# Optimization experiments

Hardware: AMD Instinct MI355X
Metric: run time of the kernel (lower is better)

Reference implementation:

```python
import jax, jax.numpy as jnp
import numpy as np

N_NODES = 100000
IN_DIM = 128
HID_DIM = 128
N_EDGES = 1600000
BN_EPS = 1e-5


def setup_inputs() -> dict:
    key = jax.random.key(0)
    k1, k2, k3, k4 = jax.random.split(key, 4)
    x = jax.random.normal(k1, (N_NODES, IN_DIM), dtype=jnp.float32)
    edge_index = jax.random.randint(k2, (2, N_EDGES), 0, N_NODES, dtype=jnp.int64)
    # GCNConv linear weight (glorot) and bias
    W = jax.random.normal(k3, (HID_DIM, IN_DIM), dtype=jnp.float32) * (1.0 / np.sqrt(IN_DIM))
    b = jnp.zeros((HID_DIM,), dtype=jnp.float32)
    # BatchNorm affine params
    gamma = jnp.ones((HID_DIM,), dtype=jnp.float32)
    beta = jnp.zeros((HID_DIM,), dtype=jnp.float32)
    return {"x": x, "edge_index": edge_index, "W": W, "b": b, "gamma": gamma, "beta": beta}


def reference(x, edge_index, W, b, gamma, beta):
    n = x.shape[0]
    # --- GCNConv: add self loops, symmetric normalization ---
    loops = jnp.arange(n, dtype=edge_index.dtype)
    row = jnp.concatenate([edge_index[0], loops])  # source j
    col = jnp.concatenate([edge_index[1], loops])  # target i
    deg = jax.ops.segment_sum(jnp.ones_like(col, dtype=x.dtype), col, num_segments=n)
    deg_inv_sqrt = jnp.where(deg > 0, jax.lax.rsqrt(jnp.maximum(deg, 1e-12)), 0.0)
    norm = deg_inv_sqrt[row] * deg_inv_sqrt[col]  # [E+N]
    # linear transform then normalized gather-scatter aggregation
    h = x @ W.T  # [N, H]
    msgs = h[row] * norm[:, None]  # [E+N, H]
    out = jax.ops.segment_sum(msgs, col, num_segments=n) + b  # [N, H]
    # --- BatchNorm1d (training-mode batch stats, biased var) + ReLU ---
    mean = jnp.mean(out, axis=0)
    var = jnp.mean(jnp.square(out - mean), axis=0)
    out = (out - mean) * jax.lax.rsqrt(var + BN_EPS) * gamma + beta
    return jax.nn.relu(out)
```

## Files before the change

### kernel.cpp

```cpp
#include <hip/hip_runtime.h>

#define N_NODES 100000
#define N_EDGES 1600000
#define BN_EPS 1e-5f
#define NB 782
#define CAP 2688
#define CH 2048

typedef short short8 __attribute__((ext_vector_type(8)));
typedef float floatx4 __attribute__((ext_vector_type(4)));

__device__ __forceinline__ unsigned short f2bf(float f) {
    unsigned int u = __float_as_uint(f);
    unsigned int r = (u + 0x7fffu + ((u >> 16) & 1u)) >> 16;
    return (unsigned short)r;
}
__device__ __forceinline__ float bflo(unsigned int v) { return __uint_as_float(v << 16); }
__device__ __forceinline__ float bfhi(unsigned int v) { return __uint_as_float(v & 0xffff0000u); }

__global__ __launch_bounds__(256) void k_bin(const int* __restrict__ ei,
                                             int* __restrict__ bcnt,
                                             unsigned int* __restrict__ binned, int E) {
    __shared__ int hist[1024];
    __shared__ int base[1024];
    __shared__ int gbase[1024];
    __shared__ int warr[256];
    __shared__ unsigned int stage[CH];
    __shared__ unsigned short stb[CH];
    int tid = threadIdx.x;
    int e0 = blockIdx.x * CH;
    int cn = min(CH, E - e0);

    for (int i = tid; i < 1024; i += 256) hist[i] = 0;
    __syncthreads();

    unsigned int mycode[8];
    short myb[8], myslot[8];
    #pragma unroll
    for (int j = 0; j < 8; j++) {
        int idx = j * 256 + tid;
        if (idx < cn) {
            int e = e0 + idx;
            int src = ei[e];
            int dst = ei[E + e];
            int b = dst >> 7;
            mycode[j] = (unsigned int)src | ((unsigned int)(dst & 127) << 17);
            myb[j] = (short)b;
            myslot[j] = (short)atomicAdd(&hist[b], 1);
        } else myb[j] = -1;
    }
    __syncthreads();

    int h0 = hist[tid * 4], h1 = hist[tid * 4 + 1], h2 = hist[tid * 4 + 2], h3 = hist[tid * 4 + 3];
    int t4 = h0 + h1 + h2 + h3;
    warr[tid] = t4;
    __syncthreads();
    for (int o = 1; o < 256; o <<= 1) {
        int x = (tid >= o) ? warr[tid - o] : 0;
        __syncthreads();
        warr[tid] += x;
        __syncthreads();
    }
    int ex = warr[tid] - t4;
    base[tid * 4] = ex;
    base[tid * 4 + 1] = ex + h0;
    base[tid * 4 + 2] = ex + h0 + h1;
    base[tid * 4 + 3] = ex + h0 + h1 + h2;
    __syncthreads();

    #pragma unroll
    for (int j = 0; j < 8; j++) {
        if (myb[j] >= 0) {
            int p = base[myb[j]] + myslot[j];
            stage[p] = mycode[j];
            stb[p] = (unsigned short)myb[j];
        }
    }
    for (int b = tid; b < NB; b += 256) {
        int c = hist[b];
        if (c) gbase[b] = b * CAP + atomicAdd(&bcnt[b], c);
    }
    __syncthreads();
    for (int i = tid; i < cn; i += 256) {
        int b = stb[i];
        binned[gbase[b] + (i - base[b])] = stage[i];
    }
}

__global__ __launch_bounds__(256) void k_dd(const unsigned int* __restrict__ binned,
                                            const int* __restrict__ bcnt,
                                            float* __restrict__ dinv, int n) {
    __shared__ int hist[128];
    int b = blockIdx.x, t = threadIdx.x;
    int nb0 = b * 128;
    int e0 = b * CAP;
    int cnt = bcnt[b];
    if (t < 128) hist[t] = 0;
    __syncthreads();
    for (int i = t; i < cnt; i += 256)
        atomicAdd(&hist[binned[e0 + i] >> 17], 1);
    __syncthreads();
    int nr = min(128, n - nb0);
    if (t < nr) dinv[nb0 + t] = rsqrtf((float)(hist[t] + 1));
}

__global__ void k_wcvt(const float* __restrict__ Wf, unsigned short* __restrict__ Wb) {
    int i = blockIdx.x * 256 + threadIdx.x;
    if (i < 128 * 128) Wb[i] = f2bf(Wf[i]);
}

__global__ __launch_bounds__(256) void k_gemm(const float* __restrict__ x,
                                              const unsigned short* __restrict__ Wb,
                                              unsigned short* __restrict__ hb, int n) {
    int w = threadIdx.x >> 6;
    int l = threadIdx.x & 63;
    int rowbase = blockIdx.x * 256 + w * 64;
    int r16 = l & 15;
    int kg = l >> 4;

    short8 a[4][4];
    #pragma unroll
    for (int m = 0; m < 4; m++) {
        int row = rowbase + m * 16 + r16;
        int rca = min(row, n - 1);
        const float* base = x + rca * 128;
        #pragma unroll
        for (int q = 0; q < 4; q++) {
            const float4* xp = (const float4*)(base + q * 32 + kg * 8);
            float4 lo = xp[0], hi = xp[1];
            short8 af;
            af[0] = (short)f2bf(lo.x); af[1] = (short)f2bf(lo.y);
            af[2] = (short)f2bf(lo.z); af[3] = (short)f2bf(lo.w);
            af[4] = (short)f2bf(hi.x); af[5] = (short)f2bf(hi.y);
            af[6] = (short)f2bf(hi.z); af[7] = (short)f2bf(hi.w);
            a[m][q] = af;
        }
    }
    for (int t = 0; t < 8; t++) {
        int col = t * 16 + r16;
        short8 b[4];
        #pragma unroll
        for (int q = 0; q < 4; q++)
            b[q] = *(const short8*)(Wb + col * 128 + q * 32 + kg * 8);

        floatx4 acc[4] = {};
        #pragma unroll
        for (int m = 0; m < 4; m++)
            #pragma unroll
            for (int q = 0; q < 4; q++)
                acc[m] = __builtin_amdgcn_mfma_f32_16x16x32_bf16(a[m][q], b[q], acc[m], 0, 0, 0);

        #pragma unroll
        for (int m = 0; m < 4; m++) {
            #pragma unroll
            for (int r = 0; r < 4; r++) {
                int row = rowbase + m * 16 + kg * 4 + r;
                if (row < n) hb[row * 128 + col] = f2bf(acc[m][r]);
            }
        }
    }
}

__global__ __launch_bounds__(512) void k_fused(const unsigned int* __restrict__ hp,
        const float* __restrict__ dinv, const int* __restrict__ bcnt,
        const unsigned int* __restrict__ binned, float* __restrict__ out,
        float* __restrict__ sums, float* __restrict__ sumsq, int n) {
    __shared__ int hist[128], hsc[128];
    __shared__ float dl[128];
    __shared__ int sh_src[CAP];
    __shared__ float sh_nrm[CAP];
    __shared__ float ps[8][128], pq[8][128];
    int t = threadIdx.x;
    int w = t >> 6, l = t & 63;
    int b = blockIdx.x;
    int nb0 = b * 128;
    int e0 = b * CAP;
    int cnt = bcnt[b];
    int nr = min(128, n - nb0);

    if (t < 128) {
        hist[t] = 0;
        if (t < nr) dl[t] = dinv[nb0 + t];
    }
    __syncthreads();

    unsigned int mycode[6];
    short myslot[6];
    #pragma unroll
    for (int j = 0; j < 6; j++) {
        int i = j * 512 + t;
        if (i < cnt) {
            unsigned int code = binned[e0 + i];
            mycode[j] = code;
            myslot[j] = (short)atomicAdd(&hist[code >> 17], 1);
        } else myslot[j] = -1;
    }
    __syncthreads();

    int v = (t < 128) ? hist[t] : 0;
    if (t < 128) hsc[t] = v;
    __syncthreads();
    for (int o = 1; o < 128; o <<= 1) {
        int x = (t < 128 && t >= o) ? hsc[t - o] : 0;
        __syncthreads();
        if (t < 128) hsc[t] += x;
        __syncthreads();
    }

    #pragma unroll
    for (int j = 0; j < 6; j++) {
        if (myslot[j] >= 0) {
            unsigned int code = mycode[j];
            int ld = code >> 17;
            int src = code & 0x1FFFF;
            int pos = hsc[ld] - hist[ld] + myslot[j];
            sh_src[pos] = src;
            sh_nrm[pos] = dinv[src] * dl[ld];
        }
    }
    __syncthreads();

    float s0 = 0, s1 = 0, q0 = 0, q1 = 0;
    for (int r = w; r < nr; r += 8) {
        int i = nb0 + r;
        float di = dl[r];
        unsigned int sv = hp[i * 64 + l];
        float sn = di * di;
        float ax = bflo(sv) * sn;
        float ay = bfhi(sv) * sn;
        int off = hsc[r] - hist[r];
        int dg = hist[r];
        int e = 0;
        for (; e + 7 < dg; e += 8) {
            unsigned int hv[8]; float nn[8];
            #pragma unroll
            for (int j = 0; j < 8; j++) {
                int s = sh_src[off + e + j];
                nn[j] = sh_nrm[off + e + j];
                hv[j] = hp[s * 64 + l];
            }
            #pragma unroll
            for (int j = 0; j < 8; j++) {
                ax += nn[j] * bflo(hv[j]);
                ay += nn[j] * bfhi(hv[j]);
            }
        }
        for (; e < dg; e++) {
            int s = sh_src[off + e];
            float nnm = sh_nrm[off + e];
            unsigned int hv = hp[s * 64 + l];
            ax += nnm * bflo(hv);
            ay += nnm * bfhi(hv);
        }
        ((float2*)out)[i * 64 + l] = make_float2(ax, ay);
        s0 += ax; q0 += ax * ax;
        s1 += ay; q1 += ay * ay;
    }

    ps[w][2 * l] = s0; ps[w][2 * l + 1] = s1;
    pq[w][2 * l] = q0; pq[w][2 * l + 1] = q1;
    __syncthreads();
    if (t < 128) {
        float s = 0, q = 0;
        #pragma unroll
        for (int j = 0; j < 8; j++) { s += ps[j][t]; q += pq[j][t]; }
        atomicAdd(&sums[t], s);
        atomicAdd(&sumsq[t], q);
    }
}

__global__ void k_bn(float* __restrict__ out, const float* __restrict__ sums,
                     const float* __restrict__ sumsq, const float* __restrict__ gamma,
                     const float* __restrict__ beta, int n) {
    int idx = blockIdx.x * 256 + threadIdx.x;
    int total = n * 32;
    if (idx >= total) return;
    int c0 = (idx & 31) * 4;
    float invN = 1.0f / (float)n;
    float4 v = ((const float4*)out)[idx];
    float r[4] = {v.x, v.y, v.z, v.w};
    #pragma unroll
    for (int j = 0; j < 4; j++) {
        int c = c0 + j;
        float mean = sums[c] * invN;
        float var = sumsq[c] * invN - mean * mean;
        float scale = rsqrtf(var + BN_EPS) * gamma[c];
        float o = (r[j] - mean) * scale + beta[c];
        r[j] = fmaxf(o, 0.0f);
    }
    ((float4*)out)[idx] = make_float4(r[0], r[1], r[2], r[3]);
}

extern "C" void kernel_launch(void* const* d_in, const int* in_sizes, int n_in,
                              void* d_out, int out_size, void* d_ws, size_t ws_size,
                              hipStream_t stream) {
    const float* x     = (const float*)d_in[0];
    const int*   ei    = (const int*)d_in[1];
    const float* W     = (const float*)d_in[2];
    const float* gamma = (const float*)d_in[4];
    const float* beta  = (const float*)d_in[5];
    float* out = (float*)d_out;

    const int n = N_NODES, E = N_EDGES;

    unsigned short* hb   = (unsigned short*)d_ws;
    float* dinv   = (float*)(hb + 12800000);
    float* sums   = dinv + 100000;
    float* sumsq  = sums + 128;
    int*   bcnt   = (int*)(sumsq + 128);
    unsigned short* Wb = (unsigned short*)(bcnt + NB);
    unsigned int* binned = (unsigned int*)(Wb + 16384);

    hipMemsetAsync(sums, 0, (256 + NB) * sizeof(int), stream);

    k_bin<<<(E + CH - 1) / CH, 256, 0, stream>>>(ei, bcnt, binned, E);
    k_dd<<<NB, 256, 0, stream>>>(binned, bcnt, dinv, n);

    k_wcvt<<<64, 256, 0, stream>>>(W, Wb);
    k_gemm<<<(n + 255) / 256, 256, 0, stream>>>(x, Wb, hb, n);

    k_fused<<<NB, 512, 0, stream>>>((const unsigned int*)hb, dinv, bcnt, binned,
                                    out, sums, sumsq, n);

    k_bn<<<(n * 32 + 255) / 256, 256, 0, stream>>>(out, sums, sumsq, gamma, beta, n);
}
```

Measured before the change: 177.3 us.

## Halve destination bin size to 64 nodes and pack edge src/norm in LDS

Destination bins shrink from 128 to 64 nodes, doubling the block count for binning, degree and fused aggregation, and the fused kernel drops to 256 threads. The GEMM processes 128 rows per block instead of 256 to launch more blocks. Source index and norm are stored together as a uint2 in shared memory so each edge takes a single LDS load. The aim is more parallelism and lower LDS use per block for better occupancy, at the cost of a larger k_bin histogram/scan and a tighter per-bin capacity that could overflow.

Result: slower. 205.6 us (+16.0%).

```diff
diff --git a/kernel.cpp b/kernel.cpp
--- a/kernel.cpp
+++ b/kernel.cpp
@@ -3,8 +3,8 @@
 #define N_NODES 100000
 #define N_EDGES 1600000
 #define BN_EPS 1e-5f
-#define NB 782
-#define CAP 2688
+#define NB 1563
+#define CAP 1472
 #define CH 2048
 
 typedef short short8 __attribute__((ext_vector_type(8)));
@@ -21,9 +21,9 @@
 __global__ __launch_bounds__(256) void k_bin(const int* __restrict__ ei,
                                              int* __restrict__ bcnt,
                                              unsigned int* __restrict__ binned, int E) {
-    __shared__ int hist[1024];
-    __shared__ int base[1024];
-    __shared__ int gbase[1024];
+    __shared__ int hist[2048];
+    __shared__ int base[2048];
+    __shared__ int gbase[2048];
     __shared__ int warr[256];
     __shared__ unsigned int stage[CH];
     __shared__ unsigned short stb[CH];
@@ -31,7 +31,7 @@
     int e0 = blockIdx.x * CH;
     int cn = min(CH, E - e0);
 
-    for (int i = tid; i < 1024; i += 256) hist[i] = 0;
+    for (int i = tid; i < 2048; i += 256) hist[i] = 0;
     __syncthreads();
 
     unsigned int mycode[8];
@@ -43,17 +43,18 @@
             int e = e0 + idx;
             int src = ei[e];
             int dst = ei[E + e];
-            int b = dst >> 7;
-            mycode[j] = (unsigned int)src | ((unsigned int)(dst & 127) << 17);
+            int b = dst >> 6;
+            mycode[j] = (unsigned int)src | ((unsigned int)(dst & 63) << 17);
             myb[j] = (short)b;
             myslot[j] = (short)atomicAdd(&hist[b], 1);
         } else myb[j] = -1;
     }
     __syncthreads();
 
-    int h0 = hist[tid * 4], h1 = hist[tid * 4 + 1], h2 = hist[tid * 4 + 2], h3 = hist[tid * 4 + 3];
-    int t4 = h0 + h1 + h2 + h3;
-    warr[tid] = t4;
+    int h[8], t8 = 0;
+    #pragma unroll
+    for (int k = 0; k < 8; k++) { h[k] = hist[tid * 8 + k]; t8 += h[k]; }
+    warr[tid] = t8;
     __syncthreads();
     for (int o = 1; o < 256; o <<= 1) {
         int x = (tid >= o) ? warr[tid - o] : 0;
@@ -61,11 +62,9 @@
         warr[tid] += x;
         __syncthreads();
     }
-    int ex = warr[tid] - t4;
-    base[tid * 4] = ex;
-    base[tid * 4 + 1] = ex + h0;
-    base[tid * 4 + 2] = ex + h0 + h1;
-    base[tid * 4 + 3] = ex + h0 + h1 + h2;
+    int ex = warr[tid] - t8;
+    #pragma unroll
+    for (int k = 0; k < 8; k++) { base[tid * 8 + k] = ex; ex += h[k]; }
     __syncthreads();
 
     #pragma unroll
@@ -90,17 +89,17 @@
 __global__ __launch_bounds__(256) void k_dd(const unsigned int* __restrict__ binned,
                                             const int* __restrict__ bcnt,
                                             float* __restrict__ dinv, int n) {
-    __shared__ int hist[128];
+    __shared__ int hist[64];
     int b = blockIdx.x, t = threadIdx.x;
-    int nb0 = b * 128;
+    int nb0 = b * 64;
     int e0 = b * CAP;
     int cnt = bcnt[b];
-    if (t < 128) hist[t] = 0;
+    if (t < 64) hist[t] = 0;
     __syncthreads();
     for (int i = t; i < cnt; i += 256)
         atomicAdd(&hist[binned[e0 + i] >> 17], 1);
     __syncthreads();
-    int nr = min(128, n - nb0);
+    int nr = min(64, n - nb0);
     if (t < nr) dinv[nb0 + t] = rsqrtf((float)(hist[t] + 1));
 }
 
@@ -114,13 +113,13 @@
                                               unsigned short* __restrict__ hb, int n) {
     int w = threadIdx.x >> 6;
     int l = threadIdx.x & 63;
-    int rowbase = blockIdx.x * 256 + w * 64;
+    int rowbase = blockIdx.x * 128 + w * 32;
     int r16 = l & 15;
     int kg = l >> 4;
 
-    short8 a[4][4];
-    #pragma unroll
-    for (int m = 0; m < 4; m++) {
+    short8 a[2][4];
+    #pragma unroll
+    for (int m = 0; m < 2; m++) {
         int row = rowbase + m * 16 + r16;
         int rca = min(row, n - 1);
         const float* base = x + rca * 128;
@@ -143,15 +142,15 @@
         for (int q = 0; q < 4; q++)
             b[q] = *(const short8*)(Wb + col * 128 + q * 32 + kg * 8);
 
-        floatx4 acc[4] = {};
-        #pragma unroll
-        for (int m = 0; m < 4; m++)
+        floatx4 acc[2] = {};
+        #pragma unroll
+        for (int m = 0; m < 2; m++)
             #pragma unroll
             for (int q = 0; q < 4; q++)
                 acc[m] = __builtin_amdgcn_mfma_f32_16x16x32_bf16(a[m][q], b[q], acc[m], 0, 0, 0);
 
         #pragma unroll
-        for (int m = 0; m < 4; m++) {
+        for (int m = 0; m < 2; m++) {
             #pragma unroll
             for (int r = 0; r < 4; r++) {
                 int row = rowbase + m * 16 + kg * 4 + r;
@@ -161,24 +160,23 @@
     }
 }
 
-__global__ __launch_bounds__(512) void k_fused(const unsigned int* __restrict__ hp,
+__global__ __launch_bounds__(256) void k_fused(const unsigned int* __restrict__ hp,
         const float* __restrict__ dinv, const int* __restrict__ bcnt,
         const unsigned int* __restrict__ binned, float* __restrict__ out,
         float* __restrict__ sums, float* __restrict__ sumsq, int n) {
-    __shared__ int hist[128], hsc[128];
-    __shared__ float dl[128];
-    __shared__ int sh_src[CAP];
-    __shared__ float sh_nrm[CAP];
-    __shared__ float ps[8][128], pq[8][128];
+    __shared__ int hist[64], hsc[64];
+    __shared__ float dl[64];
+    __shared__ uint2 sh_edge[CAP];
+    __shared__ float ps[4][128], pq[4][128];
     int t = threadIdx.x;
     int w = t >> 6, l = t & 63;
     int b = blockIdx.x;
-    int nb0 = b * 128;
+    int nb0 = b * 64;
     int e0 = b * CAP;
     int cnt = bcnt[b];
-    int nr = min(128, n - nb0);
-
-    if (t < 128) {
+    int nr = min(64, n - nb0);
+
+    if (t < 64) {
         hist[t] = 0;
         if (t < nr) dl[t] = dinv[nb0 + t];
     }
@@ -188,7 +186,7 @@
     short myslot[6];
     #pragma unroll
     for (int j = 0; j < 6; j++) {
-        int i = j * 512 + t;
+        int i = j * 256 + t;
         if (i < cnt) {
             unsigned int code = binned[e0 + i];
             mycode[j] = code;
@@ -197,13 +195,12 @@
     }
     __syncthreads();
 
-    int v = (t < 128) ? hist[t] : 0;
-    if (t < 128) hsc[t] = v;
-    __syncthreads();
-    for (int o = 1; o < 128; o <<= 1) {
-        int x = (t < 128 && t >= o) ? hsc[t - o] : 0;
+    if (t < 64) hsc[t] = hist[t];
+    __syncthreads();
+    for (int o = 1; o < 64; o <<= 1) {
+        int x = (t < 64 && t >= o) ? hsc[t - o] : 0;
         __syncthreads();
-        if (t < 128) hsc[t] += x;
+        if (t < 64) hsc[t] += x;
         __syncthreads();
     }
 
@@ -214,14 +211,14 @@
             int ld = code >> 17;
             int src = code & 0x1FFFF;
             int pos = hsc[ld] - hist[ld] + myslot[j];
-            sh_src[pos] = src;
-            sh_nrm[pos] = dinv[src] * dl[ld];
+            sh_edge[pos] = make_uint2((unsigned int)src,
+                                      __float_as_uint(dinv[src] * dl[ld]));
         }
     }
     __syncthreads();
 
     float s0 = 0, s1 = 0, q0 = 0, q1 = 0;
-    for (int r = w; r < nr; r += 8) {
+    for (int r = w; r < nr; r += 4) {
         int i = nb0 + r;
         float di = dl[r];
         unsigned int sv = hp[i * 64 + l];
@@ -235,9 +232,9 @@
             unsigned int hv[8]; float nn[8];
             #pragma unroll
             for (int j = 0; j < 8; j++) {
-                int s = sh_src[off + e + j];
-                nn[j] = sh_nrm[off + e + j];
-                hv[j] = hp[s * 64 + l];
+                uint2 ed = sh_edge[off + e + j];
+                nn[j] = __uint_as_float(ed.y);
+                hv[j] = hp[ed.x * 64 + l];
             }
             #pragma unroll
             for (int j = 0; j < 8; j++) {
@@ -246,9 +243,9 @@
             }
         }
         for (; e < dg; e++) {
-            int s = sh_src[off + e];
-            float nnm = sh_nrm[off + e];
-            unsigned int hv = hp[s * 64 + l];
+            uint2 ed = sh_edge[off + e];
+            float nnm = __uint_as_float(ed.y);
+            unsigned int hv = hp[ed.x * 64 + l];
             ax += nnm * bflo(hv);
             ay += nnm * bfhi(hv);
         }
@@ -263,7 +260,7 @@
     if (t < 128) {
         float s = 0, q = 0;
         #pragma unroll
-        for (int j = 0; j < 8; j++) { s += ps[j][t]; q += pq[j][t]; }
+        for (int j = 0; j < 4; j++) { s += ps[j][t]; q += pq[j][t]; }
         atomicAdd(&sums[t], s);
         atomicAdd(&sumsq[t], q);
     }
@@ -317,9 +314,9 @@
     k_dd<<<NB, 256, 0, stream>>>(binned, bcnt, dinv, n);
 
     k_wcvt<<<64, 256, 0, stream>>>(W, Wb);
-    k_gemm<<<(n + 255) / 256, 256, 0, stream>>>(x, Wb, hb, n);
-
-    k_fused<<<NB, 512, 0, stream>>>((const unsigned int*)hb, dinv, bcnt, binned,
+    k_gemm<<<(n + 127) / 128, 256, 0, stream>>>(x, Wb, hb, n);
+
+    k_fused<<<NB, 256, 0, stream>>>((const unsigned int*)hb, dinv, bcnt, binned,
                                     out, sums, sumsq, n);
 
     k_bn<<<(n * 32 + 255) / 256, 256, 0, stream>>>(out, sums, sumsq, gamma, beta, n);
```

## Replace single-pass edge binning with two-pass radix binning, tweak GEMM and gather

Applied to the files above, without the earlier changes.

Edge binning by destination moves from one pass over 782 fine bins to two passes: first into 25 coarse superbins of 4096 nodes, then each superbin is split into 32 sub-bins of 128 nodes. The goal is to make the global scatter writes more contiguous and cut the shared-memory histogram and scan cost of the original kernel. The GEMM now handles 128 rows per block instead of 256, which lowers register use and raises the block count. The gather kernel packs source index and norm into one uint2 in shared memory and unrolls the neighbour loop by 16 with a 4-wide tail. The extra pass adds one more kernel launch and one more round trip of the edge list through global memory.

After: 165.1 us. 6.9% less time.

```diff
diff --git a/kernel.cpp b/kernel.cpp
--- a/kernel.cpp
+++ b/kernel.cpp
@@ -3,9 +3,10 @@
 #define N_NODES 100000
 #define N_EDGES 1600000
 #define BN_EPS 1e-5f
-#define NB 782
+#define SB 25
+#define SCAP 69632
+#define NBB 800
 #define CAP 2688
-#define CH 2048
 
 typedef short short8 __attribute__((ext_vector_type(8)));
 typedef float floatx4 __attribute__((ext_vector_type(4)));
@@ -18,72 +19,107 @@
 __device__ __forceinline__ float bflo(unsigned int v) { return __uint_as_float(v << 16); }
 __device__ __forceinline__ float bfhi(unsigned int v) { return __uint_as_float(v & 0xffff0000u); }
 
-__global__ __launch_bounds__(256) void k_bin(const int* __restrict__ ei,
-                                             int* __restrict__ bcnt,
-                                             unsigned int* __restrict__ binned, int E) {
-    __shared__ int hist[1024];
-    __shared__ int base[1024];
-    __shared__ int gbase[1024];
-    __shared__ int warr[256];
-    __shared__ unsigned int stage[CH];
-    __shared__ unsigned short stb[CH];
+__global__ __launch_bounds__(512) void k_binA(const int* __restrict__ ei,
+                                              int* __restrict__ scnt,
+                                              unsigned int* __restrict__ b1, int E) {
+    __shared__ int hist[32], base[32], gbase[32];
+    __shared__ unsigned int stage[4096];
+    __shared__ unsigned char stb[4096];
     int tid = threadIdx.x;
-    int e0 = blockIdx.x * CH;
-    int cn = min(CH, E - e0);
-
-    for (int i = tid; i < 1024; i += 256) hist[i] = 0;
+    int e0 = blockIdx.x * 4096;
+    int cn = min(4096, E - e0);
+    if (tid < 32) hist[tid] = 0;
     __syncthreads();
 
     unsigned int mycode[8];
-    short myb[8], myslot[8];
+    short myslot[8];
+    signed char myb[8];
     #pragma unroll
     for (int j = 0; j < 8; j++) {
-        int idx = j * 256 + tid;
+        int idx = j * 512 + tid;
         if (idx < cn) {
-            int e = e0 + idx;
-            int src = ei[e];
-            int dst = ei[E + e];
-            int b = dst >> 7;
-            mycode[j] = (unsigned int)src | ((unsigned int)(dst & 127) << 17);
-            myb[j] = (short)b;
-            myslot[j] = (short)atomicAdd(&hist[b], 1);
+            int src = ei[e0 + idx];
+            int dst = ei[E + e0 + idx];
+            int s = dst >> 12;
+            mycode[j] = (unsigned int)src | ((unsigned int)(dst & 4095) << 17);
+            myb[j] = (signed char)s;
+            myslot[j] = (short)atomicAdd(&hist[s], 1);
         } else myb[j] = -1;
     }
     __syncthreads();
-
-    int h0 = hist[tid * 4], h1 = hist[tid * 4 + 1], h2 = hist[tid * 4 + 2], h3 = hist[tid * 4 + 3];
-    int t4 = h0 + h1 + h2 + h3;
-    warr[tid] = t4;
-    __syncthreads();
-    for (int o = 1; o < 256; o <<= 1) {
-        int x = (tid >= o) ? warr[tid - o] : 0;
-        __syncthreads();
-        warr[tid] += x;
-        __syncthreads();
-    }
-    int ex = warr[tid] - t4;
-    base[tid * 4] = ex;
-    base[tid * 4 + 1] = ex + h0;
-    base[tid * 4 + 2] = ex + h0 + h1;
-    base[tid * 4 + 3] = ex + h0 + h1 + h2;
-    __syncthreads();
-
+    if (tid == 0) {
+        int run = 0;
+        for (int s = 0; s < SB; s++) { base[s] = run; run += hist[s]; }
+    }
+    __syncthreads();
     #pragma unroll
     for (int j = 0; j < 8; j++) {
         if (myb[j] >= 0) {
             int p = base[myb[j]] + myslot[j];
             stage[p] = mycode[j];
-            stb[p] = (unsigned short)myb[j];
-        }
-    }
-    for (int b = tid; b < NB; b += 256) {
-        int c = hist[b];
-        if (c) gbase[b] = b * CAP + atomicAdd(&bcnt[b], c);
-    }
-    __syncthreads();
-    for (int i = tid; i < cn; i += 256) {
-        int b = stb[i];
-        binned[gbase[b] + (i - base[b])] = stage[i];
+            stb[p] = (unsigned char)myb[j];
+        }
+    }
+    if (tid < SB && hist[tid]) gbase[tid] = tid * SCAP + atomicAdd(&scnt[tid], hist[tid]);
+    __syncthreads();
+    for (int i = tid; i < cn; i += 512) {
+        int s = stb[i];
+        b1[gbase[s] + (i - base[s])] = stage[i];
+    }
+}
+
+__global__ __launch_bounds__(512) void k_binB(const unsigned int* __restrict__ b1,
+                                              const int* __restrict__ scnt,
+                                              int* __restrict__ bcnt,
+                                              unsigned int* __restrict__ b2) {
+    __shared__ int hist[32], base[32], gbase[32];
+    __shared__ unsigned int stage[4096];
+    __shared__ unsigned char stb[4096];
+    int tid = threadIdx.x;
+    int s = blockIdx.x / 17;
+    int c = blockIdx.x % 17;
+    int cnt = scnt[s];
+    int e0 = s * SCAP + c * 4096;
+    int cn = min(4096, cnt - c * 4096);
+    if (tid < 32) hist[tid] = 0;
+    __syncthreads();
+
+    unsigned int mycode[8];
+    short myslot[8];
+    signed char myb[8];
+    #pragma unroll
+    for (int j = 0; j < 8; j++) {
+        int idx = j * 512 + tid;
+        if (idx < cn) {
+            unsigned int code = b1[e0 + idx];
+            int sub = (code >> 24) & 31;
+            mycode[j] = code & 0x00FFFFFFu;
+            myb[j] = (signed char)sub;
+            myslot[j] = (short)atomicAdd(&hist[sub], 1);
+        } else myb[j] = -1;
+    }
+    __syncthreads();
+    if (tid == 0) {
+        int run = 0;
+        for (int k = 0; k < 32; k++) { base[k] = run; run += hist[k]; }
+    }
+    __syncthreads();
+    #pragma unroll
+    for (int j = 0; j < 8; j++) {
+        if (myb[j] >= 0) {
+            int p = base[myb[j]] + myslot[j];
+            stage[p] = mycode[j];
+            stb[p] = (unsigned char)myb[j];
+        }
+    }
+    if (tid < 32 && hist[tid]) {
+        int gb = s * 32 + tid;
+        gbase[tid] = gb * CAP + atomicAdd(&bcnt[gb], hist[tid]);
+    }
+    __syncthreads();
+    for (int i = tid; i < cn; i += 512) {
+        int sub = stb[i];
+        b2[gbase[sub] + (i - base[sub])] = stage[i];
     }
 }
 
@@ -114,13 +150,13 @@
                                               unsigned short* __restrict__ hb, int n) {
     int w = threadIdx.x >> 6;
     int l = threadIdx.x & 63;
-    int rowbase = blockIdx.x * 256 + w * 64;
+    int rowbase = blockIdx.x * 128 + w * 32;
     int r16 = l & 15;
     int kg = l >> 4;
 
-    short8 a[4][4];
-    #pragma unroll
-    for (int m = 0; m < 4; m++) {
+    short8 a[2][4];
+    #pragma unroll
+    for (int m = 0; m < 2; m++) {
         int row = rowbase + m * 16 + r16;
         int rca = min(row, n - 1);
         const float* base = x + rca * 128;
@@ -143,15 +179,15 @@
         for (int q = 0; q < 4; q++)
             b[q] = *(const short8*)(Wb + col * 128 + q * 32 + kg * 8);
 
-        floatx4 acc[4] = {};
-        #pragma unroll
-        for (int m = 0; m < 4; m++)
+        floatx4 acc[2] = {};
+        #pragma unroll
+        for (int m = 0; m < 2; m++)
             #pragma unroll
             for (int q = 0; q < 4; q++)
                 acc[m] = __builtin_amdgcn_mfma_f32_16x16x32_bf16(a[m][q], b[q], acc[m], 0, 0, 0);
 
         #pragma unroll
-        for (int m = 0; m < 4; m++) {
+        for (int m = 0; m < 2; m++) {
             #pragma unroll
             for (int r = 0; r < 4; r++) {
                 int row = rowbase + m * 16 + kg * 4 + r;
@@ -167,8 +203,7 @@
         float* __restrict__ sums, float* __restrict__ sumsq, int n) {
     __shared__ int hist[128], hsc[128];
     __shared__ float dl[128];
-    __shared__ int sh_src[CAP];
-    __shared__ float sh_nrm[CAP];
+    __shared__ uint2 sh_edge[CAP];
     __shared__ float ps[8][128], pq[8][128];
     int t = threadIdx.x;
     int w = t >> 6, l = t & 63;
@@ -214,8 +249,8 @@
             int ld = code >> 17;
             int src = code & 0x1FFFF;
             int pos = hsc[ld] - hist[ld] + myslot[j];
-            sh_src[pos] = src;
-            sh_nrm[pos] = dinv[src] * dl[ld];
+            sh_edge[pos] = make_uint2((unsigned int)src,
+                                      __float_as_uint(dinv[src] * dl[ld]));
         }
     }
     __syncthreads();
@@ -231,24 +266,38 @@
         int off = hsc[r] - hist[r];
         int dg = hist[r];
         int e = 0;
-        for (; e + 7 < dg; e += 8) {
-            unsigned int hv[8]; float nn[8];
-            #pragma unroll
-            for (int j = 0; j < 8; j++) {
-                int s = sh_src[off + e + j];
-                nn[j] = sh_nrm[off + e + j];
-                hv[j] = hp[s * 64 + l];
-            }
-            #pragma unroll
-            for (int j = 0; j < 8; j++) {
+        for (; e + 15 < dg; e += 16) {
+            unsigned int hv[16]; float nn[16];
+            #pragma unroll
+            for (int j = 0; j < 16; j++) {
+                uint2 ed = sh_edge[off + e + j];
+                nn[j] = __uint_as_float(ed.y);
+                hv[j] = hp[ed.x * 64 + l];
+            }
+            #pragma unroll
+            for (int j = 0; j < 16; j++) {
                 ax += nn[j] * bflo(hv[j]);
                 ay += nn[j] * bfhi(hv[j]);
             }
         }
+        for (; e + 3 < dg; e += 4) {
+            unsigned int hv[4]; float nn[4];
+            #pragma unroll
+            for (int j = 0; j < 4; j++) {
+                uint2 ed = sh_edge[off + e + j];
+                nn[j] = __uint_as_float(ed.y);
+                hv[j] = hp[ed.x * 64 + l];
+            }
+            #pragma unroll
+            for (int j = 0; j < 4; j++) {
+                ax += nn[j] * bflo(hv[j]);
+                ay += nn[j] * bfhi(hv[j]);
+            }
+        }
         for (; e < dg; e++) {
-            int s = sh_src[off + e];
-            float nnm = sh_nrm[off + e];
-            unsigned int hv = hp[s * 64 + l];
+            uint2 ed = sh_edge[off + e];
+            float nnm = __uint_as_float(ed.y);
+            unsigned int hv = hp[ed.x * 64 + l];
             ax += nnm * bflo(hv);
             ay += nnm * bfhi(hv);
         }
@@ -308,19 +357,22 @@
     float* sums   = dinv + 100000;
     float* sumsq  = sums + 128;
     int*   bcnt   = (int*)(sumsq + 128);
-    unsigned short* Wb = (unsigned short*)(bcnt + NB);
-    unsigned int* binned = (unsigned int*)(Wb + 16384);
-
-    hipMemsetAsync(sums, 0, (256 + NB) * sizeof(int), stream);
-
-    k_bin<<<(E + CH - 1) / CH, 256, 0, stream>>>(ei, bcnt, binned, E);
-    k_dd<<<NB, 256, 0, stream>>>(binned, bcnt, dinv, n);
+    int*   scnt   = bcnt + NBB;
+    unsigned short* Wb = (unsigned short*)(scnt + SB);
+    unsigned int* b1 = (unsigned int*)(Wb + 16384);
+    unsigned int* b2 = b1 + SB * SCAP;
+
+    hipMemsetAsync(sums, 0, (256 + NBB + SB) * sizeof(int), stream);
+
+    k_binA<<<(E + 4095) / 4096, 512, 0, stream>>>(ei, scnt, b1, E);
+    k_binB<<<SB * 17, 512, 0, stream>>>(b1, scnt, bcnt, b2);
+    k_dd<<<NBB, 256, 0, stream>>>(b2, bcnt, dinv, n);
 
     k_wcvt<<<64, 256, 0, stream>>>(W, Wb);
-    k_gemm<<<(n + 255) / 256, 256, 0, stream>>>(x, Wb, hb, n);
-
-    k_fused<<<NB, 512, 0, stream>>>((const unsigned int*)hb, dinv, bcnt, binned,
-                                    out, sums, sumsq, n);
+    k_gemm<<<(n + 127) / 128, 256, 0, stream>>>(x, Wb, hb, n);
+
+    k_fused<<<NBB, 512, 0, stream>>>((const unsigned int*)hb, dinv, bcnt, b2,
+                                     out, sums, sumsq, n);
 
     k_bn<<<(n * 32 + 255) / 256, 256, 0, stream>>>(out, sums, sumsq, gamma, beta, n);
 }
```
